# Performance work log

Hardware: AMD Instinct MI355X
Metric: run time of the kernel (lower is better)

## Reference

```python
import jax, jax.numpy as jnp
import numpy as np

UNITS = 65536  # shape[0] * shape[1]
S0, S1 = 256, 256
BOND = 32
IN_DIM = 2     # forced by the original code's reshape([vec, vec], (2, 2))
BATCH = 2048


def setup_inputs() -> dict:
    key = jax.random.key(0)
    k_in, k_c1, k_c2 = jax.random.split(key, 3)
    inputs = jax.random.normal(k_in, (BATCH, IN_DIM), dtype=jnp.float32)
    # core_1: (input_dim, shape[0], bond), core_2: (input_dim, shape[1], bond)
    core1 = jax.random.normal(k_c1, (IN_DIM, S0, BOND), dtype=jnp.float32) * 0.05
    core2 = jax.random.normal(k_c2, (IN_DIM, S1, BOND), dtype=jnp.float32) * 0.05
    bias = jnp.zeros((S0, S1), dtype=jnp.float32)
    return {"inputs": inputs, "core1": core1, "core2": core2, "bias": bias}


def reference(inputs, core1, core2, bias):
    # Original per-sample op: x = reshape([vec, vec], (2,2)) so x[i, j] = vec[j];
    # ncon: result[a, c] = sum_{i,j,p} x[i,j] * core1[i,a,p] * core2[j,c,p]
    # Batched over all samples in one einsum (replaces tf.vectorized_map + ncon).
    X = jnp.stack([inputs, inputs], axis=1)            # (B, 2, 2), rows identical
    res = jnp.einsum('bij,iap,jcp->bac', X, core1, core2)  # (B, S0, S1)
    res = res + bias                                    # broadcast bias (S0, S1)
    return jax.nn.relu(res.reshape(-1, UNITS))          # (B, units)
```

## Files before the change

kernel.cpp:

```cpp
#include <hip/hip_runtime.h>

#define S0d   256
#define S1d   256
#define BONDd 32
#define BATCHd 2048
#define UNITSd 65536
#define UCHUNK 1024
#define BCHUNK 64

__global__ __launch_bounds__(256) void precompute_G(
    const float* __restrict__ core1, const float* __restrict__ core2,
    float* __restrict__ G) {
  const int u = blockIdx.x * 256 + threadIdx.x;
  const int a = u >> 8;
  const int c = u & 255;
  const float4* c10 = (const float4*)(core1 + a * BONDd);
  const float4* c11 = (const float4*)(core1 + S0d * BONDd + a * BONDd);
  const float4* r0  = (const float4*)(core2 + c * BONDd);
  const float4* r1  = (const float4*)(core2 + S1d * BONDd + c * BONDd);
  float acc0 = 0.f, acc1 = 0.f;
#pragma unroll
  for (int q = 0; q < BONDd / 4; ++q) {
    float4 x = c10[q], y = c11[q];
    float sx = x.x + y.x, sy = x.y + y.y, sz = x.z + y.z, sw = x.w + y.w;
    float4 v0 = r0[q], v1 = r1[q];
    acc0 = fmaf(sx, v0.x, fmaf(sy, v0.y, fmaf(sz, v0.z, fmaf(sw, v0.w, acc0))));
    acc1 = fmaf(sx, v1.x, fmaf(sy, v1.y, fmaf(sz, v1.z, fmaf(sw, v1.w, acc1))));
  }
  G[u] = acc0;
  G[UNITSd + u] = acc1;
}

__global__ __launch_bounds__(256) void td_main(
    const float* __restrict__ inputs, const float* __restrict__ G,
    const float* __restrict__ bias, float* __restrict__ out) {
  const int u = blockIdx.x * UCHUNK + threadIdx.x * 4;
  const float4 g0 = *(const float4*)(G + u);
  const float4 g1 = *(const float4*)(G + UNITSd + u);
  const float4 bs = *(const float4*)(bias + u);
  const int b0 = blockIdx.y * BCHUNK;
  float* outp = out + (size_t)b0 * UNITSd + u;
#pragma unroll 4
  for (int k = 0; k < BCHUNK; ++k) {
    const float2 x = *(const float2*)(inputs + (b0 + k) * 2);
    float4 r;
    r.x = fmaxf(fmaf(x.y, g1.x, fmaf(x.x, g0.x, bs.x)), 0.f);
    r.y = fmaxf(fmaf(x.y, g1.y, fmaf(x.x, g0.y, bs.y)), 0.f);
    r.z = fmaxf(fmaf(x.y, g1.z, fmaf(x.x, g0.z, bs.z)), 0.f);
    r.w = fmaxf(fmaf(x.y, g1.w, fmaf(x.x, g0.w, bs.w)), 0.f);
    *(float4*)outp = r;
    outp += UNITSd;
  }
}

__global__ __launch_bounds__(256) void td_fused(
    const float* __restrict__ inputs, const float* __restrict__ core1,
    const float* __restrict__ core2, const float* __restrict__ bias,
    float* __restrict__ out) {
  const int u = blockIdx.x * UCHUNK + threadIdx.x * 4;
  const int a = u >> 8;
  const int c = u & 255;
  float s[BONDd];
#pragma unroll
  for (int p = 0; p < BONDd; ++p)
    s[p] = core1[a * BONDd + p] + core1[S0d * BONDd + a * BONDd + p];
  float g0[4], g1[4];
#pragma unroll
  for (int cc = 0; cc < 4; ++cc) {
    float a0 = 0.f, a1 = 0.f;
#pragma unroll
    for (int p = 0; p < BONDd; ++p) {
      a0 = fmaf(s[p], core2[(c + cc) * BONDd + p], a0);
      a1 = fmaf(s[p], core2[S1d * BONDd + (c + cc) * BONDd + p], a1);
    }
    g0[cc] = a0; g1[cc] = a1;
  }
  const float4 bs = *(const float4*)(bias + u);
  const int b0 = blockIdx.y * BCHUNK;
  float* outp = out + (size_t)b0 * UNITSd + u;
#pragma unroll 4
  for (int k = 0; k < BCHUNK; ++k) {
    const float2 x = *(const float2*)(inputs + (b0 + k) * 2);
    float4 r;
    r.x = fmaxf(fmaf(x.y, g1[0], fmaf(x.x, g0[0], bs.x)), 0.f);
    r.y = fmaxf(fmaf(x.y, g1[1], fmaf(x.x, g0[1], bs.y)), 0.f);
    r.z = fmaxf(fmaf(x.y, g1[2], fmaf(x.x, g0[2], bs.z)), 0.f);
    r.w = fmaxf(fmaf(x.y, g1[3], fmaf(x.x, g0[3], bs.w)), 0.f);
    *(float4*)outp = r;
    outp += UNITSd;
  }
}

extern "C" void kernel_launch(void* const* d_in, const int* in_sizes, int n_in,
                              void* d_out, int out_size, void* d_ws, size_t ws_size,
                              hipStream_t stream) {
  const float* inputs = (const float*)d_in[0];
  const float* core1  = (const float*)d_in[1];
  const float* core2  = (const float*)d_in[2];
  const float* bias   = (const float*)d_in[3];
  float* out = (float*)d_out;

  const size_t g_bytes = (size_t)2 * UNITSd * sizeof(float);
  if (ws_size >= g_bytes) {
    float* G = (float*)d_ws;
    precompute_G<<<UNITSd / 256, 256, 0, stream>>>(core1, core2, G);
    td_main<<<dim3(UNITSd / UCHUNK, BATCHd / BCHUNK), 256, 0, stream>>>(
        inputs, G, bias, out);
  } else {
    td_fused<<<dim3(UNITSd / UCHUNK, BATCHd / BCHUNK), 256, 0, stream>>>(
        inputs, core1, core2, bias, out);
  }
}
```

Baseline: 120.3 us.

## Write one output row per block with nontemporal stores

Replaces the batch-chunked main kernel with a kernel where each block handles a single batch row. It streams G and bias through the full row and writes contiguous output using nontemporal stores. The goal is to reduce cache pollution and improve write streaming for the large output. In exchange, G and bias are re-read from cache for every row.

```diff
diff --git a/kernel.cpp b/kernel.cpp
--- a/kernel.cpp
+++ b/kernel.cpp
@@ -5,8 +5,9 @@
 #define BONDd 32
 #define BATCHd 2048
 #define UNITSd 65536
-#define UCHUNK 1024
-#define BCHUNK 64
+
+typedef float f32x4 __attribute__((ext_vector_type(4)));
+typedef float f32x2 __attribute__((ext_vector_type(2)));
 
 __global__ __launch_bounds__(256) void precompute_G(
     const float* __restrict__ core1, const float* __restrict__ core2,
@@ -14,42 +15,42 @@
   const int u = blockIdx.x * 256 + threadIdx.x;
   const int a = u >> 8;
   const int c = u & 255;
-  const float4* c10 = (const float4*)(core1 + a * BONDd);
-  const float4* c11 = (const float4*)(core1 + S0d * BONDd + a * BONDd);
-  const float4* r0  = (const float4*)(core2 + c * BONDd);
-  const float4* r1  = (const float4*)(core2 + S1d * BONDd + c * BONDd);
+  const f32x4* c10 = (const f32x4*)(core1 + a * BONDd);
+  const f32x4* c11 = (const f32x4*)(core1 + S0d * BONDd + a * BONDd);
+  const f32x4* r0  = (const f32x4*)(core2 + c * BONDd);
+  const f32x4* r1  = (const f32x4*)(core2 + S1d * BONDd + c * BONDd);
   float acc0 = 0.f, acc1 = 0.f;
 #pragma unroll
   for (int q = 0; q < BONDd / 4; ++q) {
-    float4 x = c10[q], y = c11[q];
-    float sx = x.x + y.x, sy = x.y + y.y, sz = x.z + y.z, sw = x.w + y.w;
-    float4 v0 = r0[q], v1 = r1[q];
-    acc0 = fmaf(sx, v0.x, fmaf(sy, v0.y, fmaf(sz, v0.z, fmaf(sw, v0.w, acc0))));
-    acc1 = fmaf(sx, v1.x, fmaf(sy, v1.y, fmaf(sz, v1.z, fmaf(sw, v1.w, acc1))));
+    f32x4 x = c10[q], y = c11[q];
+    f32x4 s = x + y;
+    f32x4 v0 = r0[q], v1 = r1[q];
+    acc0 = fmaf(s.x, v0.x, fmaf(s.y, v0.y, fmaf(s.z, v0.z, fmaf(s.w, v0.w, acc0))));
+    acc1 = fmaf(s.x, v1.x, fmaf(s.y, v1.y, fmaf(s.z, v1.z, fmaf(s.w, v1.w, acc1))));
   }
   G[u] = acc0;
   G[UNITSd + u] = acc1;
 }
 
-__global__ __launch_bounds__(256) void td_main(
+__global__ __launch_bounds__(256) void td_row(
     const float* __restrict__ inputs, const float* __restrict__ G,
     const float* __restrict__ bias, float* __restrict__ out) {
-  const int u = blockIdx.x * UCHUNK + threadIdx.x * 4;
-  const float4 g0 = *(const float4*)(G + u);
-  const float4 g1 = *(const float4*)(G + UNITSd + u);
-  const float4 bs = *(const float4*)(bias + u);
-  const int b0 = blockIdx.y * BCHUNK;
-  float* outp = out + (size_t)b0 * UNITSd + u;
+  const int b = blockIdx.x;
+  const f32x2 x = *(const f32x2*)(inputs + b * 2);
+  float* outp = out + (size_t)b * UNITSd;
+  const int base = threadIdx.x * 4;
 #pragma unroll 4
-  for (int k = 0; k < BCHUNK; ++k) {
-    const float2 x = *(const float2*)(inputs + (b0 + k) * 2);
-    float4 r;
+  for (int it = 0; it < UNITSd / 1024; ++it) {
+    const int u = it * 1024 + base;
+    const f32x4 g0 = *(const f32x4*)(G + u);
+    const f32x4 g1 = *(const f32x4*)(G + UNITSd + u);
+    const f32x4 bs = *(const f32x4*)(bias + u);
+    f32x4 r;
     r.x = fmaxf(fmaf(x.y, g1.x, fmaf(x.x, g0.x, bs.x)), 0.f);
     r.y = fmaxf(fmaf(x.y, g1.y, fmaf(x.x, g0.y, bs.y)), 0.f);
     r.z = fmaxf(fmaf(x.y, g1.z, fmaf(x.x, g0.z, bs.z)), 0.f);
     r.w = fmaxf(fmaf(x.y, g1.w, fmaf(x.x, g0.w, bs.w)), 0.f);
-    *(float4*)outp = r;
-    outp += UNITSd;
+    __builtin_nontemporal_store(r, (f32x4*)(outp + u));
   }
 }
 
@@ -57,7 +58,7 @@
     const float* __restrict__ inputs, const float* __restrict__ core1,
     const float* __restrict__ core2, const float* __restrict__ bias,
     float* __restrict__ out) {
-  const int u = blockIdx.x * UCHUNK + threadIdx.x * 4;
+  const int u = blockIdx.x * 1024 + threadIdx.x * 4;
   const int a = u >> 8;
   const int c = u & 255;
   float s[BONDd];
@@ -75,18 +76,18 @@
     }
     g0[cc] = a0; g1[cc] = a1;
   }
-  const float4 bs = *(const float4*)(bias + u);
-  const int b0 = blockIdx.y * BCHUNK;
+  const f32x4 bs = *(const f32x4*)(bias + u);
+  const int b0 = blockIdx.y * 64;
   float* outp = out + (size_t)b0 * UNITSd + u;
 #pragma unroll 4
-  for (int k = 0; k < BCHUNK; ++k) {
-    const float2 x = *(const float2*)(inputs + (b0 + k) * 2);
-    float4 r;
+  for (int k = 0; k < 64; ++k) {
+    const f32x2 x = *(const f32x2*)(inputs + (b0 + k) * 2);
+    f32x4 r;
     r.x = fmaxf(fmaf(x.y, g1[0], fmaf(x.x, g0[0], bs.x)), 0.f);
     r.y = fmaxf(fmaf(x.y, g1[1], fmaf(x.x, g0[1], bs.y)), 0.f);
     r.z = fmaxf(fmaf(x.y, g1[2], fmaf(x.x, g0[2], bs.z)), 0.f);
     r.w = fmaxf(fmaf(x.y, g1[3], fmaf(x.x, g0[3], bs.w)), 0.f);
-    *(float4*)outp = r;
+    *(f32x4*)outp = r;
     outp += UNITSd;
   }
 }
@@ -104,10 +105,9 @@
   if (ws_size >= g_bytes) {
     float* G = (float*)d_ws;
     precompute_G<<<UNITSd / 256, 256, 0, stream>>>(core1, core2, G);
-    td_main<<<dim3(UNITSd / UCHUNK, BATCHd / BCHUNK), 256, 0, stream>>>(
-        inputs, G, bias, out);
+    td_row<<<BATCHd, 256, 0, stream>>>(inputs, G, bias, out);
   } else {
-    td_fused<<<dim3(UNITSd / UCHUNK, BATCHd / BCHUNK), 256, 0, stream>>>(
+    td_fused<<<dim3(UNITSd / 1024, BATCHd / 64), 256, 0, stream>>>(
         inputs, core1, core2, bias, out);
   }
 }
```

Measured after the change: 111.1 us. -7.6%, faster.
